# Optimization experiments

Hardware: AMD Instinct MI355X
Metric: run time of the kernel (lower is better)

## Reference

```python
import jax, jax.numpy as jnp
import numpy as np

N = 50000   # nodes
E = 1000000 # edges
D = 64      # input_dim
H = 64      # hidden dim (both hidden layers)
O = 16      # output_dim
G = 512     # number of graphs in the batch


def setup_inputs() -> dict:
    key = jax.random.key(0)
    ks = jax.random.split(key, 12)
    s = 0.05
    x = jax.random.normal(ks[0], (N, D), dtype=jnp.float32)
    edge_index = jax.random.randint(ks[1], (2, E), 0, N, dtype=jnp.int32)
    batch = jnp.sort(jax.random.randint(ks[2], (N,), 0, G, dtype=jnp.int32))
    # SAGEConv layer 1: lin_l (neighbor aggregate, with bias), lin_r (root, no bias)
    Wl1 = jax.random.normal(ks[3], (D, H), dtype=jnp.float32) * s
    Wr1 = jax.random.normal(ks[4], (D, H), dtype=jnp.float32) * s
    b1 = jnp.zeros((H,), dtype=jnp.float32)
    # SAGEConv layer 2
    Wl2 = jax.random.normal(ks[5], (H, H), dtype=jnp.float32) * s
    Wr2 = jax.random.normal(ks[6], (H, H), dtype=jnp.float32) * s
    b2 = jnp.zeros((H,), dtype=jnp.float32)
    # final Linear head
    Wo = jax.random.normal(ks[7], (H, O), dtype=jnp.float32) * s
    bo = jnp.zeros((O,), dtype=jnp.float32)
    return {"x": x, "edge_index": edge_index, "batch": batch,
            "Wl1": Wl1, "Wr1": Wr1, "b1": b1,
            "Wl2": Wl2, "Wr2": Wr2, "b2": b2,
            "Wo": Wo, "bo": bo}


def reference(x, edge_index, batch, Wl1, Wr1, b1, Wl2, Wr2, b2, Wo, bo):
    src, dst = edge_index[0], edge_index[1]  # source_to_target message flow

    def sage(h, Wl, Wr, b):
        # aggr='add': sum messages x_j from src into dst, then
        # out = lin_l(aggr) + lin_r(h)   (PyG SAGEConv, bias on lin_l)
        agg = jax.ops.segment_sum(h[src], dst, num_segments=N)  # [N, d]
        return agg @ Wl + h @ Wr + b

    h = jax.nn.relu(sage(x, Wl1, Wr1, b1))
    h = jax.nn.relu(sage(h, Wl2, Wr2, b2))
    g = jax.ops.segment_sum(h, batch, num_segments=G)  # global_add_pool -> [G, H]
    # dropout is identity in eval mode
    return g @ Wo + bo  # [G, O]
```

## Files before the change

kernel.cpp:

```cpp
#include <hip/hip_runtime.h>


namespace {
constexpr int NN = 50000;
constexpr int NE = 1000000;
constexpr int NG = 512;
constexpr int NO = 16;
constexpr int KB = 196;
constexpr int BCAP = 10240;
constexpr int EPT = 8;
constexpr int EPB = 256 * EPT;
constexpr int SBLK = (NE + EPB - 1) / EPB;
constexpr int SEDGE = BCAP;
constexpr int CVT_BLK = (NN * 64 / 8 + 255) / 256;
constexpr int WP_BLK = 64;
}

typedef __attribute__((ext_vector_type(8))) short bf16x8;
typedef __attribute__((ext_vector_type(4))) float f32x4;
typedef __attribute__((ext_vector_type(2))) float f32x2;

__device__ __forceinline__ unsigned short f2bf(float f) {
  unsigned u = __float_as_uint(f);
  u += 0x7FFFu + ((u >> 16) & 1u);
  return (unsigned short)(u >> 16);
}

__device__ __forceinline__ unsigned char f2fp8(float f) {
  return (unsigned char)(__builtin_amdgcn_cvt_pk_fp8_f32(f, f, 0, false) &
                         0xFF);
}

__device__ __forceinline__ bf16x8 f8x8_to_bf16(uint2 u) {
  f32x2 l0 = __builtin_amdgcn_cvt_pk_f32_fp8(u.x, false);
  f32x2 l1 = __builtin_amdgcn_cvt_pk_f32_fp8(u.x, true);
  f32x2 l2 = __builtin_amdgcn_cvt_pk_f32_fp8(u.y, false);
  f32x2 l3 = __builtin_amdgcn_cvt_pk_f32_fp8(u.y, true);
  bf16x8 r;
  r[0] = (short)f2bf(l0.x);
  r[1] = (short)f2bf(l0.y);
  r[2] = (short)f2bf(l1.x);
  r[3] = (short)f2bf(l1.y);
  r[4] = (short)f2bf(l2.x);
  r[5] = (short)f2bf(l2.y);
  r[6] = (short)f2bf(l3.x);
  r[7] = (short)f2bf(l3.y);
  return r;
}

__global__ __launch_bounds__(256) void prep_all(
    const float* __restrict__ x, unsigned char* __restrict__ x_f8,
    const float* __restrict__ Wl1, const float* __restrict__ Wr1,
    const float* __restrict__ Wl2, const float* __restrict__ Wr2,
    unsigned short* __restrict__ Wt1, unsigned short* __restrict__ Wt2,
    const int* __restrict__ ei, int* __restrict__ bcount,
    unsigned int* __restrict__ ebuf) {
  __shared__ unsigned int stage[EPB];
  __shared__ int cnt[256];
  __shared__ int lbase[256];
  __shared__ int cur[256];
  __shared__ int gbase[256];
  __shared__ int total_sh;
  int b = blockIdx.x;
  int t = threadIdx.x;

  if (b < CVT_BLK) {
    int i = b * 256 + t;
    if (i >= NN * 8) return;
    const float4* p = reinterpret_cast<const float4*>(x) + (size_t)i * 2;
    float4 a = p[0], bb = p[1];
    unsigned lo = __builtin_amdgcn_cvt_pk_fp8_f32(a.x, a.y, 0, false);
    lo = __builtin_amdgcn_cvt_pk_fp8_f32(a.z, a.w, lo, true);
    unsigned hi = __builtin_amdgcn_cvt_pk_fp8_f32(bb.x, bb.y, 0, false);
    hi = __builtin_amdgcn_cvt_pk_fp8_f32(bb.z, bb.w, hi, true);
    uint2 u8;
    u8.x = lo;
    u8.y = hi;
    reinterpret_cast<uint2*>(x_f8)[i] = u8;
    return;
  }
  if (b < CVT_BLK + WP_BLK) {
    int id = (b - CVT_BLK) * 256 + t;
    int half = id >> 13;
    int e = id & 8191;
    int nrow = e >> 7;
    int kk = e & 127;
    const float* Wl = half ? Wl2 : Wl1;
    const float* Wr = half ? Wr2 : Wr1;
    unsigned short* Wt = half ? Wt2 : Wt1;
    float v = (kk < 64) ? Wl[kk * 64 + nrow] : Wr[(kk - 64) * 64 + nrow];
    Wt[nrow * 128 + kk] = f2bf(v);
    return;
  }
  int sb = b - (CVT_BLK + WP_BLK);
  cnt[t] = 0;
  __syncthreads();
  int e0 = sb * EPB;
  unsigned int pk[EPT];
#pragma unroll
  for (int i = 0; i < EPT; ++i) {
    int e = e0 + i * 256 + t;
    if (e < NE) {
      unsigned int src = (unsigned int)ei[e];
      unsigned int dst = (unsigned int)ei[NE + e];
      pk[i] = (dst << 16) | src;
      atomicAdd(&cnt[dst >> 8], 1);
    } else {
      pk[i] = 0xFFFFFFFFu;
    }
  }
  __syncthreads();
  int deg = cnt[t];
  for (int off = 1; off < 256; off <<= 1) {
    int u = (t >= off) ? cnt[t - off] : 0;
    __syncthreads();
    cnt[t] += u;
    __syncthreads();
  }
  {
    int excl = cnt[t] - deg;
    lbase[t] = excl;
    cur[t] = excl;
    if (t < KB) gbase[t] = t * BCAP + atomicAdd(&bcount[t], deg);
    if (t == 255) total_sh = cnt[255];
  }
  __syncthreads();
#pragma unroll
  for (int i = 0; i < EPT; ++i) {
    if (pk[i] != 0xFFFFFFFFu) {
      int bb2 = pk[i] >> 24;
      int s = atomicAdd(&cur[bb2], 1);
      stage[s] = pk[i];
    }
  }
  __syncthreads();
  int total = total_sh;
  for (int s = t; s < total; s += 256) {
    unsigned int p = stage[s];
    int bb2 = p >> 24;
    ebuf[gbase[bb2] + (s - lbase[bb2])] = p;
  }
}

__global__ __launch_bounds__(512) void bucket_sort(
    const unsigned int* __restrict__ ebuf, const int* __restrict__ bcount,
    unsigned int* __restrict__ meta, unsigned short* __restrict__ col) {
  __shared__ unsigned int se[SEDGE];
  __shared__ int cnt[256];
  __shared__ int cur[256];
  int b = blockIdx.x;
  int t = threadIdx.x;
  int n = bcount[b];
  const unsigned int* eb = ebuf + (size_t)b * BCAP;
  if (t < 256) cnt[t] = 0;
  __syncthreads();
  for (int j = t; j < n; j += 512) {
    unsigned int p = eb[j];
    se[j] = p;
    atomicAdd(&cnt[(p >> 16) & 255], 1);
  }
  __syncthreads();
  int deg = (t < 256) ? cnt[t] : 0;
  for (int off = 1; off < 256; off <<= 1) {
    int u = (t >= off && t < 256) ? cnt[t - off] : 0;
    __syncthreads();
    if (t < 256) cnt[t] += u;
    __syncthreads();
  }
  if (t < 256) {
    int excl = cnt[t] - deg;
    cur[t] = excl;
    int node = (b << 8) + t;
    if (node < NN) {
      meta[node] = ((unsigned)(b * BCAP + excl) << 11) | (unsigned)deg;
    }
  }
  __syncthreads();
  unsigned short* cb = col + (size_t)b * BCAP;
  for (int j = t; j < n; j += 512) {
    unsigned int p = se[j];
    int d = (p >> 16) & 255;
    int pos = atomicAdd(&cur[d], 1);
    cb[pos] = (unsigned short)(p & 0xFFFFu);
  }
}

template <bool POOL>
__global__ __launch_bounds__(256) void sage_fused(
    const unsigned char* __restrict__ feat8,
    const unsigned int* __restrict__ meta, const unsigned short* __restrict__ col,
    const unsigned short* __restrict__ Wt, const float* __restrict__ bias,
    unsigned char* __restrict__ out8, const int* __restrict__ batch,
    float* __restrict__ pooled) {
  __shared__ __align__(16) unsigned short tile[16][72];
  __shared__ float psm[16][64];
  int tid = threadIdx.x;
  int wave = tid >> 6;
  int lane = tid & 63;
  long base = (long)blockIdx.x * 16;

  int r = lane >> 4;
  int h = (lane >> 3) & 1;
  int o = lane & 7;
  long row = base + wave * 4 + r;
  unsigned int md = meta[row];

  int m = lane & 15;
  int q = lane >> 4;
  const uint2* f8b = reinterpret_cast<const uint2*>(feat8);
  uint2 rt0 = f8b[(base + m) * 8 + q];
  uint2 rt1 = f8b[(base + m) * 8 + 4 + q];
  float bv = bias[wave * 16 + m];

  {
    int beg = (int)(md >> 11);
    int deg = (int)(md & 2047u);
    int T = (deg - h + 1) >> 1;
    const uint2* fb = f8b;
    const unsigned short* cp = col + beg + h;
    float a0 = 0.f, a1 = 0.f, a2 = 0.f, a3 = 0.f;
    float a4 = 0.f, a5 = 0.f, a6 = 0.f, a7 = 0.f;

    auto ACC = [&](uint2 u) {
      f32x2 l0 = __builtin_amdgcn_cvt_pk_f32_fp8(u.x, false);
      f32x2 l1 = __builtin_amdgcn_cvt_pk_f32_fp8(u.x, true);
      f32x2 l2 = __builtin_amdgcn_cvt_pk_f32_fp8(u.y, false);
      f32x2 l3 = __builtin_amdgcn_cvt_pk_f32_fp8(u.y, true);
      a0 += l0.x;
      a1 += l0.y;
      a2 += l1.x;
      a3 += l1.y;
      a4 += l2.x;
      a5 += l2.y;
      a6 += l3.x;
      a7 += l3.y;
    };

    int s0 = cp[0];
    int s1 = cp[(1 < T ? 1 : 0) * 2];
    int s2 = cp[(2 < T ? 2 : 0) * 2];
    int s3 = cp[(3 < T ? 3 : 0) * 2];
    uint2 u0 = fb[(size_t)s0 * 8 + o];
    uint2 u1 = fb[(size_t)s1 * 8 + o];
    uint2 u2 = fb[(size_t)s2 * 8 + o];
    uint2 u3 = fb[(size_t)s3 * 8 + o];

    for (int k = 0; k < T; k += 4) {
      int i4 = (k + 4 < T) ? (k + 4) : 0;
      int i5 = (k + 5 < T) ? (k + 5) : 0;
      int i6 = (k + 6 < T) ? (k + 6) : 0;
      int i7 = (k + 7 < T) ? (k + 7) : 0;
      int t0 = cp[i4 * 2];
      int t1 = cp[i5 * 2];
      int t2 = cp[i6 * 2];
      int t3 = cp[i7 * 2];
      uint2 v0 = fb[(size_t)t0 * 8 + o];
      uint2 v1 = fb[(size_t)t1 * 8 + o];
      uint2 v2 = fb[(size_t)t2 * 8 + o];
      uint2 v3 = fb[(size_t)t3 * 8 + o];
      ACC(u0);
      if (k + 1 < T) ACC(u1);
      if (k + 2 < T) ACC(u2);
      if (k + 3 < T) ACC(u3);
      u0 = v0;
      u1 = v1;
      u2 = v2;
      u3 = v3;
    }

    a0 += __shfl_xor(a0, 8);
    a1 += __shfl_xor(a1, 8);
    a2 += __shfl_xor(a2, 8);
    a3 += __shfl_xor(a3, 8);
    a4 += __shfl_xor(a4, 8);
    a5 += __shfl_xor(a5, 8);
    a6 += __shfl_xor(a6, 8);
    a7 += __shfl_xor(a7, 8);
    if (h == 0) {
      uint4 pk;
      pk.x = (unsigned)f2bf(a0) | ((unsigned)f2bf(a1) << 16);
      pk.y = (unsigned)f2bf(a2) | ((unsigned)f2bf(a3) << 16);
      pk.z = (unsigned)f2bf(a4) | ((unsigned)f2bf(a5) << 16);
      pk.w = (unsigned)f2bf(a6) | ((unsigned)f2bf(a7) << 16);
      *reinterpret_cast<uint4*>(&tile[wave * 4 + r][o * 8]) = pk;
    }
  }

  bf16x8 af2 = f8x8_to_bf16(rt0);
  bf16x8 af3 = f8x8_to_bf16(rt1);
  __syncthreads();

  bf16x8 af0 = *reinterpret_cast<const bf16x8*>(&tile[m][q * 8]);
  bf16x8 af1 = *reinterpret_cast<const bf16x8*>(&tile[m][32 + q * 8]);
  f32x4 acc;
  acc[0] = bv;
  acc[1] = bv;
  acc[2] = bv;
  acc[3] = bv;
  const unsigned short* wrow = Wt + (size_t)(wave * 16 + m) * 128 + q * 8;
  acc = __builtin_amdgcn_mfma_f32_16x16x32_bf16(
      af0, *(const bf16x8*)(wrow + 0), acc, 0, 0, 0);
  acc = __builtin_amdgcn_mfma_f32_16x16x32_bf16(
      af1, *(const bf16x8*)(wrow + 32), acc, 0, 0, 0);
  acc = __builtin_amdgcn_mfma_f32_16x16x32_bf16(
      af2, *(const bf16x8*)(wrow + 64), acc, 0, 0, 0);
  acc = __builtin_amdgcn_mfma_f32_16x16x32_bf16(
      af3, *(const bf16x8*)(wrow + 96), acc, 0, 0, 0);

  if (POOL) {
#pragma unroll
    for (int r2 = 0; r2 < 4; ++r2) {
      psm[q * 4 + r2][wave * 16 + m] = fmaxf(acc[r2], 0.f);
    }
    __syncthreads();
    if (tid < 64) {
      int c = tid;
      float run = 0.f;
      int g = batch[base];
      for (int i = 0; i < 16; ++i) {
        int gi = batch[base + i];
        if (gi != g) {
          atomicAdd(&pooled[(size_t)g * 64 + c], run);
          run = 0.f;
          g = gi;
        }
        run += psm[i][c];
      }
      atomicAdd(&pooled[(size_t)g * 64 + c], run);
    }
  } else {
#pragma unroll
    for (int r2 = 0; r2 < 4; ++r2) {
      float v = fmaxf(acc[r2], 0.f);
      long rowc = base + q * 4 + r2;
      out8[rowc * 64 + wave * 16 + m] = f2fp8(v);
    }
  }
}

__global__ __launch_bounds__(256) void head_kernel(
    const float* __restrict__ pooled, const float* __restrict__ Wo,
    const float* __restrict__ bo, float* __restrict__ out) {
  int id = blockIdx.x * 256 + threadIdx.x;
  if (id >= NG * NO) return;
  int g = id >> 4, o = id & 15;
  float acc = bo[o];
  const float* p = pooled + (size_t)g * 64;
#pragma unroll
  for (int k = 0; k < 64; ++k) acc += p[k] * Wo[k * 16 + o];
  out[id] = acc;
}

extern "C" void kernel_launch(void* const* d_in, const int* in_sizes, int n_in,
                              void* d_out, int out_size, void* d_ws,
                              size_t ws_size, hipStream_t stream) {
  const float* x = (const float*)d_in[0];
  const int* ei = (const int*)d_in[1];
  const int* batch = (const int*)d_in[2];
  const float* Wl1 = (const float*)d_in[3];
  const float* Wr1 = (const float*)d_in[4];
  const float* b1 = (const float*)d_in[5];
  const float* Wl2 = (const float*)d_in[6];
  const float* Wr2 = (const float*)d_in[7];
  const float* b2 = (const float*)d_in[8];
  const float* Wo = (const float*)d_in[9];
  const float* bo = (const float*)d_in[10];
  float* out = (float*)d_out;

  unsigned char* x_f8 = (unsigned char*)d_ws;
  unsigned char* h1_f8 = x_f8 + (size_t)NN * 64;
  unsigned short* col = (unsigned short*)(h1_f8 + (size_t)NN * 64);
  unsigned short* Wt1 = col + (size_t)KB * BCAP;
  unsigned short* Wt2 = Wt1 + 64 * 128;
  unsigned int* ebuf = (unsigned int*)(Wt2 + 64 * 128);
  unsigned int* meta = ebuf + (size_t)KB * BCAP;
  int* bcount = (int*)(meta + NN);
  float* pooled = (float*)(bcount + KB);

  hipMemsetAsync(bcount, 0, KB * sizeof(int) + (size_t)NG * 64 * sizeof(float),
                 stream);

  const int fused_blocks = NN / 16;

  prep_all<<<CVT_BLK + WP_BLK + SBLK, 256, 0, stream>>>(
      x, x_f8, Wl1, Wr1, Wl2, Wr2, Wt1, Wt2, ei, bcount, ebuf);

  bucket_sort<<<KB, 512, 0, stream>>>(ebuf, bcount, meta, col);

  sage_fused<false><<<fused_blocks, 256, 0, stream>>>(
      x_f8, meta, col, Wt1, b1, h1_f8, batch, pooled);

  sage_fused<true><<<fused_blocks, 256, 0, stream>>>(
      h1_f8, meta, col, Wt2, b2, nullptr, batch, pooled);

  head_kernel<<<(NG * NO + 255) / 256, 256, 0, stream>>>(pooled, Wo, bo, out);
}
```

Before: 151.7 us.

## Merge both SAGE layers and head into one persistent cooperative kernel

Replaces the three launches (layer 1, layer 2, head) with a single cooperative persistent kernel. Blocks loop over 16-row tiles and use grid.sync between phases. The aim is to remove launch gaps and the tail of each separate kernel. In exchange it adds grid-wide barriers, extra __syncthreads per tile, and a grid size limited by occupancy (assumes 256 CUs), which may lower latency hiding compared with the previous one-block-per-tile launch.

Measured after the change: 387.6 us. +155.5%, slower.

```diff
diff --git a/kernel.cpp b/kernel.cpp
--- a/kernel.cpp
+++ b/kernel.cpp
@@ -1,4 +1,7 @@
 #include <hip/hip_runtime.h>
+#include <hip/hip_cooperative_groups.h>
+
+namespace cg = cooperative_groups;
 
 
 namespace {
@@ -14,6 +17,7 @@
 constexpr int SEDGE = BCAP;
 constexpr int CVT_BLK = (NN * 64 / 8 + 255) / 256;
 constexpr int WP_BLK = 64;
+constexpr int NTILE = NN / 16;
 }
 
 typedef __attribute__((ext_vector_type(8))) short bf16x8;
@@ -186,18 +190,18 @@
 }
 
 template <bool POOL>
-__global__ __launch_bounds__(256) void sage_fused(
-    const unsigned char* __restrict__ feat8,
-    const unsigned int* __restrict__ meta, const unsigned short* __restrict__ col,
+__device__ __forceinline__ void sage_tile(
+    int tileIdx, const unsigned char* __restrict__ feat8,
+    const unsigned int* __restrict__ meta,
+    const unsigned short* __restrict__ col,
     const unsigned short* __restrict__ Wt, const float* __restrict__ bias,
     unsigned char* __restrict__ out8, const int* __restrict__ batch,
-    float* __restrict__ pooled) {
-  __shared__ __align__(16) unsigned short tile[16][72];
-  __shared__ float psm[16][64];
+    float* __restrict__ pooled, unsigned short tile[16][72],
+    float psm[16][64]) {
   int tid = threadIdx.x;
   int wave = tid >> 6;
   int lane = tid & 63;
-  long base = (long)blockIdx.x * 16;
+  long base = (long)tileIdx * 16;
 
   int r = lane >> 4;
   int h = (lane >> 3) & 1;
@@ -336,6 +340,75 @@
       out8[rowc * 64 + wave * 16 + m] = f2fp8(v);
     }
   }
+  __syncthreads();
+}
+
+__global__ __launch_bounds__(256, 4) void sage_all(
+    const unsigned char* __restrict__ x_f8, unsigned char* __restrict__ h1_f8,
+    const unsigned int* __restrict__ meta,
+    const unsigned short* __restrict__ col,
+    const unsigned short* __restrict__ Wt1, const float* __restrict__ b1,
+    const unsigned short* __restrict__ Wt2, const float* __restrict__ b2,
+    const int* __restrict__ batch, float* __restrict__ pooled,
+    const float* __restrict__ Wo, const float* __restrict__ bo,
+    float* __restrict__ out) {
+  __shared__ __align__(16) unsigned short tile[16][72];
+  __shared__ float psm[16][64];
+  cg::grid_group grid = cg::this_grid();
+  int nb = gridDim.x;
+
+  for (int t = blockIdx.x; t < NTILE; t += nb) {
+    sage_tile<false>(t, x_f8, meta, col, Wt1, b1, h1_f8, batch, pooled, tile,
+                     psm);
+  }
+  __threadfence();
+  grid.sync();
+
+  for (int t = blockIdx.x; t < NTILE; t += nb) {
+    sage_tile<true>(t, h1_f8, meta, col, Wt2, b2, nullptr, batch, pooled, tile,
+                    psm);
+  }
+  __threadfence();
+  grid.sync();
+
+  int id = blockIdx.x * 256 + threadIdx.x;
+  if (id < NG * NO) {
+    int g = id >> 4, oo = id & 15;
+    float acc = bo[oo];
+    const float* p = pooled + (size_t)g * 64;
+#pragma unroll
+    for (int k = 0; k < 64; ++k) acc += p[k] * Wo[k * 16 + oo];
+    out[id] = acc;
+  }
+}
+
+__global__ __launch_bounds__(256) void sage_layer1(
+    const unsigned char* __restrict__ feat8,
+    const unsigned int* __restrict__ meta,
+    const unsigned short* __restrict__ col,
+    const unsigned short* __restrict__ Wt, const float* __restrict__ bias,
+    unsigned char* __restrict__ out8, const int* __restrict__ batch,
+    float* __restrict__ pooled) {
+  __shared__ __align__(16) unsigned short tile[16][72];
+  __shared__ float psm[16][64];
+  for (int t = blockIdx.x; t < NTILE; t += gridDim.x) {
+    sage_tile<false>(t, feat8, meta, col, Wt, bias, out8, batch, pooled, tile,
+                     psm);
+  }
+}
+
+__global__ __launch_bounds__(256) void sage_layer2(
+    const unsigned char* __restrict__ feat8,
+    const unsigned int* __restrict__ meta,
+    const unsigned short* __restrict__ col,
+    const unsigned short* __restrict__ Wt, const float* __restrict__ bias,
+    const int* __restrict__ batch, float* __restrict__ pooled) {
+  __shared__ __align__(16) unsigned short tile[16][72];
+  __shared__ float psm[16][64];
+  for (int t = blockIdx.x; t < NTILE; t += gridDim.x) {
+    sage_tile<true>(t, feat8, meta, col, Wt, bias, nullptr, batch, pooled,
+                    tile, psm);
+  }
 }
 
 __global__ __launch_bounds__(256) void head_kernel(
@@ -380,18 +453,47 @@
   hipMemsetAsync(bcount, 0, KB * sizeof(int) + (size_t)NG * 64 * sizeof(float),
                  stream);
 
-  const int fused_blocks = NN / 16;
-
   prep_all<<<CVT_BLK + WP_BLK + SBLK, 256, 0, stream>>>(
       x, x_f8, Wl1, Wr1, Wl2, Wr2, Wt1, Wt2, ei, bcount, ebuf);
 
   bucket_sort<<<KB, 512, 0, stream>>>(ebuf, bcount, meta, col);
 
-  sage_fused<false><<<fused_blocks, 256, 0, stream>>>(
-      x_f8, meta, col, Wt1, b1, h1_f8, batch, pooled);
-
-  sage_fused<true><<<fused_blocks, 256, 0, stream>>>(
-      h1_f8, meta, col, Wt2, b2, nullptr, batch, pooled);
-
-  head_kernel<<<(NG * NO + 255) / 256, 256, 0, stream>>>(pooled, Wo, bo, out);
-}
+  static int coopGrid = 0;
+  if (coopGrid == 0) {
+    int perCU = 0;
+    hipError_t oe = hipOccupancyMaxActiveBlocksPerMultiprocessor(
+        &perCU, (const void*)sage_all, 256, 0);
+    if (oe != hipSuccess || perCU < 1) perCU = 4;
+    long g = (long)perCU * 256;
+    if (g > NTILE) g = NTILE;
+    coopGrid = (int)g;
+  }
+
+  {
+    const unsigned char* a0 = x_f8;
+    unsigned char* a1 = h1_f8;
+    const unsigned int* a2 = meta;
+    const unsigned short* a3 = col;
+    const unsigned short* a4 = Wt1;
+    const float* a5 = b1;
+    const unsigned short* a6 = Wt2;
+    const float* a7 = b2;
+    const int* a8 = batch;
+    float* a9 = pooled;
+    const float* a10 = Wo;
+    const float* a11 = bo;
+    float* a12 = out;
+    void* args[] = {&a0, &a1, &a2, &a3, &a4, &a5, &a6,
+                    &a7, &a8, &a9, &a10, &a11, &a12};
+    hipError_t err = hipLaunchCooperativeKernel(
+        (const void*)sage_all, dim3(coopGrid), dim3(256), args, 0, stream);
+    if (err != hipSuccess) {
+      sage_layer1<<<NTILE, 256, 0, stream>>>(x_f8, meta, col, Wt1, b1, h1_f8,
+                                             batch, pooled);
+      sage_layer2<<<NTILE, 256, 0, stream>>>(h1_f8, meta, col, Wt2, b2, batch,
+                                             pooled);
+      head_kernel<<<(NG * NO + 255) / 256, 256, 0, stream>>>(pooled, Wo, bo,
+                                                             out);
+    }
+  }
+}
```
